# Optimization experiments

Measured on AMD Instinct MI355X. Metric: run time of the kernel, lower is better.

Reference implementation:

```python
import jax, jax.numpy as jnp
import numpy as np

N_NODES = 100000

def _sage(x, src, tgt, Wl, bl, Wr):
    # PyG SAGEConv (mean aggr): out = lin_l(mean_{j in N(i)} x_j) + lin_r(x_i)
    msg = x[src]                                             # [E, F] gather
    s = jax.ops.segment_sum(msg, tgt, num_segments=N_NODES)  # [N, F]
    cnt = jax.ops.segment_sum(jnp.ones((src.shape[0], 1), x.dtype), tgt, num_segments=N_NODES)
    agg = s / jnp.maximum(cnt, 1.0)
    return agg @ Wl + bl + x @ Wr


def setup_inputs() -> dict:
    key = jax.random.key(0)
    ks = jax.random.split(key, 16)
    node_dim, edge_dim, hidden = 128, 16, 64
    E = 1000000
    x = jax.random.normal(ks[0], (N_NODES, node_dim), jnp.float32)
    edge_index = jax.random.randint(ks[1], (2, E), 0, N_NODES, jnp.int64)
    edge_attr = jax.random.normal(ks[2], (E, edge_dim), jnp.float32)
    def lin(k, fi, fo, scale=None):
        s = scale if scale is not None else 1.0 / np.sqrt(fi)
        return jax.random.uniform(k, (fi, fo), jnp.float32, -s, s)
    return {
        "x": x, "edge_index": edge_index, "edge_attr": edge_attr,
        # edge MLP: Linear(16,64) -> ReLU -> Linear(64,64)
        "We1": lin(ks[3], edge_dim, hidden), "be1": jnp.zeros((hidden,), jnp.float32),
        "We2": lin(ks[4], hidden, hidden),   "be2": jnp.zeros((hidden,), jnp.float32),
        # SAGEConv 0: lin_l (with bias, on aggregated) + lin_r (no bias, on root)
        "Wl0": lin(ks[5], node_dim, hidden), "bl0": jnp.zeros((hidden,), jnp.float32),
        "Wr0": lin(ks[6], node_dim, hidden),
        # SAGEConv 1
        "Wl1": lin(ks[7], hidden, hidden), "bl1": jnp.zeros((hidden,), jnp.float32),
        "Wr1": lin(ks[8], hidden, hidden),
        # output MLP: Linear(64,64) -> ReLU -> (Dropout eval=id) -> Linear(64,1)
        "Wo1": lin(ks[9], hidden, hidden), "bo1": jnp.zeros((hidden,), jnp.float32),
        "Wo2": lin(ks[10], hidden, 1),     "bo2": jnp.zeros((1,), jnp.float32),
    }


def reference(x, edge_index, edge_attr, We1, be1, We2, be2,
              Wl0, bl0, Wr0, Wl1, bl1, Wr1, Wo1, bo1, Wo2, bo2):
    src, tgt = edge_index[0], edge_index[1]
    # edge MLP (dropout in eval mode = identity)
    ea = jax.nn.relu(edge_attr @ We1 + be1) @ We2 + be2       # [E, H]
    # two SAGE layers with ReLU
    h = jax.nn.relu(_sage(x, src, tgt, Wl0, bl0, Wr0))        # [N, H]
    h = jax.nn.relu(_sage(h, src, tgt, Wl1, bl1, Wr1))        # [N, H]
    # per-edge features: gather both endpoints + edge embedding
    ef = h[src] + h[tgt] + ea                                 # [E, H]
    out = jax.nn.relu(ef @ Wo1 + bo1) @ Wo2 + bo2             # [E, 1]
    return jax.nn.sigmoid(out[:, 0])                          # [E]
```

## Files before the change

kernel.cpp:

```cpp
#include <hip/hip_runtime.h>
#include <math.h>

typedef __attribute__((ext_vector_type(8))) short short8;
typedef __attribute__((ext_vector_type(4))) float f32x4;

static __device__ __forceinline__ unsigned short f2bf(float f) {
  union { float f; unsigned int u; } x; x.f = f;
  unsigned int r = x.u + 0x7fffu + ((x.u >> 16) & 1u);
  return (unsigned short)(r >> 16);
}
static __device__ __forceinline__ float bf2f(unsigned int u) {
  union { unsigned int u; float f; } x; x.u = u << 16; return x.f;
}

__global__ void k_flag(const unsigned int* __restrict__ w, int nSample,
                       unsigned int* __restrict__ flag) {
  __shared__ unsigned int red[256];
  unsigned int v = 0;
  for (int i = threadIdx.x; i < nSample; i += 256) v |= w[2 * i + 1];
  red[threadIdx.x] = v;
  __syncthreads();
  for (int s = 128; s > 0; s >>= 1) {
    if (threadIdx.x < s) red[threadIdx.x] |= red[threadIdx.x + s];
    __syncthreads();
  }
  if (threadIdx.x == 0) flag[0] = red[0];
}

__global__ void k_decode(const unsigned int* __restrict__ w,
                         const unsigned int* __restrict__ flag, int E,
                         int* __restrict__ src, int* __restrict__ tgt,
                         int* __restrict__ posin, int* __restrict__ deg) {
  int e = blockIdx.x * 256 + threadIdx.x;
  if (e >= E) return;
  int s, t;
  if (flag[0]) { s = (int)w[e]; t = (int)w[E + e]; }
  else         { s = (int)w[2 * e]; t = (int)w[2 * (E + e)]; }
  src[e] = s;
  tgt[e] = t;
  posin[e] = atomicAdd(deg + t, 1);
}

__global__ __launch_bounds__(256) void k_scan1(const int* __restrict__ deg,
                                               int* __restrict__ bsum) {
  __shared__ int wsum[4];
  const int tid = threadIdx.x, lane = tid & 63, wid = tid >> 6;
  const int base = blockIdx.x * 2048 + tid * 8;
  int4 v0 = *(const int4*)(deg + base);
  int4 v1 = *(const int4*)(deg + base + 4);
  int s = v0.x + v0.y + v0.z + v0.w + v1.x + v1.y + v1.z + v1.w;
#pragma unroll
  for (int off = 1; off < 64; off <<= 1) s += __shfl_xor(s, off, 64);
  if (lane == 0) wsum[wid] = s;
  __syncthreads();
  if (tid == 0) bsum[blockIdx.x] = wsum[0] + wsum[1] + wsum[2] + wsum[3];
}

__global__ void k_scan2(const int* __restrict__ bsum, int* __restrict__ boff,
                        int nB, int* __restrict__ rowptrN) {
  int lane = threadIdx.x;
  int v = (lane < nB) ? bsum[lane] : 0;
  int incl = v;
#pragma unroll
  for (int off = 1; off < 64; off <<= 1) {
    int t = __shfl_up(incl, off, 64);
    if (lane >= off) incl += t;
  }
  if (lane < nB) boff[lane] = incl - v;
  if (lane == 63) *rowptrN = incl;
}

__global__ __launch_bounds__(256) void k_scan3(const int* __restrict__ deg,
                                               const int* __restrict__ boff,
                                               int* __restrict__ rowptr) {
  __shared__ int wsum[4];
  const int tid = threadIdx.x, lane = tid & 63, wid = tid >> 6;
  const int base = blockIdx.x * 2048 + tid * 8;
  int4 v0 = *(const int4*)(deg + base);
  int4 v1 = *(const int4*)(deg + base + 4);
  int e[8] = {v0.x, v0.y, v0.z, v0.w, v1.x, v1.y, v1.z, v1.w};
  int s = e[0] + e[1] + e[2] + e[3] + e[4] + e[5] + e[6] + e[7];
  int incl = s;
#pragma unroll
  for (int off = 1; off < 64; off <<= 1) {
    int t = __shfl_up(incl, off, 64);
    if (lane >= off) incl += t;
  }
  if (lane == 63) wsum[wid] = incl;
  __syncthreads();
  int run = boff[blockIdx.x] + (incl - s);
  for (int w = 0; w < wid; ++w) run += wsum[w];
  int o[8];
#pragma unroll
  for (int i = 0; i < 8; ++i) { o[i] = run; run += e[i]; }
  *(int4*)(rowptr + base) = make_int4(o[0], o[1], o[2], o[3]);
  *(int4*)(rowptr + base + 4) = make_int4(o[4], o[5], o[6], o[7]);
}

__global__ void k_fill(const int* __restrict__ src, const int* __restrict__ tgt,
                       const int* __restrict__ posin,
                       const int* __restrict__ rowptr,
                       int* __restrict__ csrc, int E) {
  int e = blockIdx.x * 256 + threadIdx.x;
  if (e >= E) return;
  csrc[rowptr[tgt[e]] + posin[e]] = src[e];
}

template <int K>
__global__ void k_prep2(const float* __restrict__ W0,
                        const float* __restrict__ W1,
                        unsigned short* __restrict__ WnT) {
  int idx = blockIdx.x * 256 + threadIdx.x;
  if (idx >= 128 * K) return;
  int n = idx / K, k = idx % K;
  float v = (n < 64) ? W0[(size_t)k * 64 + n] : W1[(size_t)k * 64 + (n - 64)];
  WnT[idx] = f2bf(v);
}

template <int K, bool BF16IN, int NTILES>
__global__ __launch_bounds__(256) void k_ngemm(
    const void* __restrict__ Xv, const unsigned short* __restrict__ WnT,
    unsigned short* __restrict__ Y0, unsigned short* __restrict__ Y1, int N) {
  constexpr int STR = K + 8;
  constexpr int NC = K / 32;
  __shared__ unsigned short sX[64 * STR];
  const int tid = threadIdx.x;
  const int wv = tid >> 6, lane = tid & 63;
  const int m = lane & 15, q = lane >> 4;
  const int row0 = blockIdx.x * 64;

  short8 bB[NTILES][NC];
#pragma unroll
  for (int ct = 0; ct < NTILES; ++ct)
#pragma unroll
    for (int c = 0; c < NC; ++c) {
      int n = (NTILES == 2) ? (wv * 32 + ct * 16 + m) : (wv * 16 + m);
      bB[ct][c] = *(const short8*)(WnT + (size_t)n * K + c * 32 + q * 8);
    }

#pragma unroll
  for (int i = 0; i < K / 16; ++i) {
    int f = tid + 256 * i;
    int r = f / (K / 4);
    int c4 = f % (K / 4);
    int rr = row0 + r; if (rr >= N) rr = N - 1;
    uint2 pk;
    if constexpr (BF16IN) {
      pk = *(const uint2*)((const unsigned short*)Xv + (size_t)rr * K + c4 * 4);
    } else {
      float4 v = *(const float4*)((const float*)Xv + (size_t)rr * K + c4 * 4);
      pk.x = (unsigned int)f2bf(v.x) | ((unsigned int)f2bf(v.y) << 16);
      pk.y = (unsigned int)f2bf(v.z) | ((unsigned int)f2bf(v.w) << 16);
    }
    *(uint2*)(sX + r * STR + c4 * 4) = pk;
  }
  __syncthreads();

  f32x4 acc[4][NTILES];
#pragma unroll
  for (int rt = 0; rt < 4; ++rt)
#pragma unroll
    for (int ct = 0; ct < NTILES; ++ct)
#pragma unroll
      for (int r = 0; r < 4; ++r) acc[rt][ct][r] = 0.f;

#pragma unroll
  for (int c = 0; c < NC; ++c) {
    short8 a[4];
#pragma unroll
    for (int rt = 0; rt < 4; ++rt)
      a[rt] = *(const short8*)(sX + (rt * 16 + m) * STR + c * 32 + q * 8);
#pragma unroll
    for (int rt = 0; rt < 4; ++rt)
#pragma unroll
      for (int ct = 0; ct < NTILES; ++ct)
        acc[rt][ct] = __builtin_amdgcn_mfma_f32_16x16x32_bf16(a[rt], bB[ct][c], acc[rt][ct], 0, 0, 0);
  }

#pragma unroll
  for (int rt = 0; rt < 4; ++rt)
#pragma unroll
    for (int ct = 0; ct < NTILES; ++ct) {
      unsigned short* Yw;
      int n;
      if constexpr (NTILES == 2) {
        Yw = (wv < 2) ? Y0 : Y1;
        n = (wv & 1) * 32 + ct * 16 + m;
      } else {
        Yw = Y0;
        n = wv * 16 + m;
      }
#pragma unroll
      for (int reg = 0; reg < 4; ++reg) {
        int row = row0 + rt * 16 + q * 4 + reg;
        if (row < N) Yw[(size_t)row * 64 + n] = f2bf(acc[rt][ct][reg]);
      }
    }
}

__global__ __launch_bounds__(256) void k_prep(
    const float* __restrict__ We2, const float* __restrict__ Wo1,
    const float* __restrict__ be2, const float* __restrict__ bo1,
    const float* __restrict__ We1,
    unsigned short* __restrict__ W25T, unsigned short* __restrict__ We1T,
    unsigned short* __restrict__ Wo1T, float* __restrict__ cvec) {
  __shared__ float sA[4096];
  __shared__ float sB[4096];
  int tid = threadIdx.x;
  for (int i = tid; i < 1024; i += 256) {
    *(float4*)&sA[i * 4] = *(const float4*)(We2 + i * 4);
    *(float4*)&sB[i * 4] = *(const float4*)(Wo1 + i * 4);
  }
  __syncthreads();
  for (int idx = tid; idx < 4096; idx += 256) {
    int n = idx >> 6, k = idx & 63;
    float s = 0.f;
#pragma unroll 8
    for (int mm = 0; mm < 64; ++mm) s = fmaf(sA[k * 64 + mm], sB[mm * 64 + n], s);
    W25T[idx] = f2bf(s);
    Wo1T[idx] = f2bf(sB[k * 64 + n]);
  }
  for (int idx = tid; idx < 2048; idx += 256) {
    int n = idx >> 5, k = idx & 31;
    We1T[n * 32 + k] = (k < 16) ? f2bf(We1[k * 64 + n]) : (unsigned short)0;
  }
  if (tid < 64) {
    float s = bo1[tid];
#pragma unroll 8
    for (int mm = 0; mm < 64; ++mm) s = fmaf(be2[mm], sB[mm * 64 + tid], s);
    cvec[tid] = s;
  }
}

__global__ __launch_bounds__(256) void k_agg(
    const unsigned short* __restrict__ Y, const int* __restrict__ rowptr,
    const int* __restrict__ csrc, const float* __restrict__ bias,
    const unsigned short* __restrict__ Yr, unsigned short* __restrict__ H,
    int N) {
  int node = (blockIdx.x * 256 + threadIdx.x) >> 6;
  if (node >= N) return;
  const int lane = threadIdx.x & 63;
  const int c4 = lane & 15, rr = lane >> 4;
  int beg = rowptr[node], end = rowptr[node + 1];
  float a0 = 0.f, a1 = 0.f, a2 = 0.f, a3 = 0.f;
  float b0 = 0.f, b1 = 0.f, b2 = 0.f, b3 = 0.f;
  for (int e = beg; e < end; e += 8) {
    int e0 = e + rr, e1 = e + 4 + rr;
    if (e0 < end) {
      int s = csrc[e0];
      uint2 v = *(const uint2*)(Y + (size_t)s * 64 + c4 * 4);
      a0 += bf2f(v.x & 0xffffu); a1 += bf2f(v.x >> 16);
      a2 += bf2f(v.y & 0xffffu); a3 += bf2f(v.y >> 16);
    }
    if (e1 < end) {
      int s = csrc[e1];
      uint2 v = *(const uint2*)(Y + (size_t)s * 64 + c4 * 4);
      b0 += bf2f(v.x & 0xffffu); b1 += bf2f(v.x >> 16);
      b2 += bf2f(v.y & 0xffffu); b3 += bf2f(v.y >> 16);
    }
  }
  a0 += b0; a1 += b1; a2 += b2; a3 += b3;
#pragma unroll
  for (int msk = 16; msk <= 32; msk <<= 1) {
    a0 += __shfl_xor(a0, msk, 64);
    a1 += __shfl_xor(a1, msk, 64);
    a2 += __shfl_xor(a2, msk, 64);
    a3 += __shfl_xor(a3, msk, 64);
  }
  if (rr == 0) {
    float cdeg = (float)(end - beg);
    if (cdeg < 1.f) cdeg = 1.f;
    float inv = 1.f / cdeg;
    float4 bv = *(const float4*)(bias + c4 * 4);
    uint2 yv = *(const uint2*)(Yr + (size_t)node * 64 + c4 * 4);
    float o0 = fmaxf(a0 * inv + bv.x + bf2f(yv.x & 0xffffu), 0.f);
    float o1 = fmaxf(a1 * inv + bv.y + bf2f(yv.x >> 16), 0.f);
    float o2 = fmaxf(a2 * inv + bv.z + bf2f(yv.y & 0xffffu), 0.f);
    float o3 = fmaxf(a3 * inv + bv.w + bf2f(yv.y >> 16), 0.f);
    uint2 pk;
    pk.x = (unsigned int)f2bf(o0) | ((unsigned int)f2bf(o1) << 16);
    pk.y = (unsigned int)f2bf(o2) | ((unsigned int)f2bf(o3) << 16);
    *(uint2*)(H + (size_t)node * 64 + c4 * 4) = pk;
  }
}

#define T1_STRIDE 72
#define G_STRIDE 68
__global__ __launch_bounds__(256) void k_edge3(
    const float* __restrict__ eattr, const int* __restrict__ src,
    const int* __restrict__ tgt, const unsigned short* __restrict__ Gb,
    const unsigned short* __restrict__ We1T,
    const unsigned short* __restrict__ W25T,
    const float* __restrict__ cvec, const float* __restrict__ be1,
    const float* __restrict__ Wo2, const float* __restrict__ bo2,
    float* __restrict__ out, int E, int nT, int nWaves) {
  __shared__ unsigned short sT1a[4][16 * T1_STRIDE];
  __shared__ float sGa[4][16 * G_STRIDE];
  const int tid = threadIdx.x;
  const int wid = tid >> 6, lane = tid & 63;
  const int m = lane & 15, q = lane >> 4;
  unsigned short* sT1 = sT1a[wid];
  float* sG = sGa[wid];

  short8 bWe1[4], bW25[4][2];
  float cv[4], wo2v[4], be1v[4];
#pragma unroll
  for (int nt = 0; nt < 4; ++nt) {
    int n = nt * 16 + m;
    bWe1[nt] = *(const short8*)(We1T + n * 32 + q * 8);
    bW25[nt][0] = *(const short8*)(W25T + n * 64 + q * 8);
    bW25[nt][1] = *(const short8*)(W25T + n * 64 + 32 + q * 8);
    cv[nt] = cvec[n];
    wo2v[nt] = Wo2[n];
    be1v[nt] = be1[n];
  }
  const float b_out = bo2[0];
  const short8 zfrag = {};

  int t = blockIdx.x * 4 + wid;
  if (t >= nT) return;
  int il = t * 16 + m; if (il >= E) il = E - 1;
  int my_idx = (lane < 16) ? src[il] : ((lane < 32) ? tgt[il] : 0);

  while (true) {
    const int base = t * 16;
    const int tn = t + nWaves;
    const bool last = (tn >= nT);
    const int tc = last ? t : tn;

    int il_n = tc * 16 + m; if (il_n >= E) il_n = E - 1;
    int idx_n = (lane < 16) ? src[il_n] : ((lane < 32) ? tgt[il_n] : 0);

    int rs[4], rt[4];
#pragma unroll
    for (int r = 0; r < 4; ++r) {
      rs[r] = __shfl(my_idx, q * 4 + r, 64);
      rt[r] = __shfl(my_idx, 16 + q * 4 + r, 64);
    }
    uint2 sv[4], tv[4];
#pragma unroll
    for (int r = 0; r < 4; ++r) {
      sv[r] = *(const uint2*)(Gb + (size_t)rs[r] * 64 + m * 4);
      tv[r] = *(const uint2*)(Gb + (size_t)rt[r] * 64 + m * 4);
    }

    int er = base + m; if (er >= E) er = E - 1;
    const float* ep = eattr + (size_t)er * 16 + (q & 1) * 8;
    float4 e0 = *(const float4*)ep;
    float4 e1 = *(const float4*)(ep + 4);
    short8 aEA;
    {
      union { short8 s; unsigned int u[4]; } ua;
      ua.u[0] = (unsigned int)f2bf(e0.x) | ((unsigned int)f2bf(e0.y) << 16);
      ua.u[1] = (unsigned int)f2bf(e0.z) | ((unsigned int)f2bf(e0.w) << 16);
      ua.u[2] = (unsigned int)f2bf(e1.x) | ((unsigned int)f2bf(e1.y) << 16);
      ua.u[3] = (unsigned int)f2bf(e1.z) | ((unsigned int)f2bf(e1.w) << 16);
      aEA = (q < 2) ? ua.s : zfrag;
    }

    f32x4 t1[4];
#pragma unroll
    for (int nt = 0; nt < 4; ++nt) {
      f32x4 cinit; cinit[0] = be1v[nt]; cinit[1] = be1v[nt];
      cinit[2] = be1v[nt]; cinit[3] = be1v[nt];
      t1[nt] = __builtin_amdgcn_mfma_f32_16x16x32_bf16(aEA, bWe1[nt], cinit, 0, 0, 0);
    }
#pragma unroll
    for (int nt = 0; nt < 4; ++nt)
#pragma unroll
      for (int r = 0; r < 4; ++r)
        sT1[(q * 4 + r) * T1_STRIDE + nt * 16 + m] = f2bf(fmaxf(t1[nt][r], 0.f));
    short8 aT0 = *(short8*)(sT1 + m * T1_STRIDE + q * 8);
    short8 aT1 = *(short8*)(sT1 + m * T1_STRIDE + 32 + q * 8);

#pragma unroll
    for (int r = 0; r < 4; ++r) {
      f32x4 g;
      g[0] = bf2f(sv[r].x & 0xffffu) + bf2f(tv[r].x & 0xffffu);
      g[1] = bf2f(sv[r].x >> 16)     + bf2f(tv[r].x >> 16);
      g[2] = bf2f(sv[r].y & 0xffffu) + bf2f(tv[r].y & 0xffffu);
      g[3] = bf2f(sv[r].y >> 16)     + bf2f(tv[r].y >> 16);
      *(f32x4*)(sG + (q * 4 + r) * G_STRIDE + m * 4) = g;
    }

    f32x4 acc[4];
#pragma unroll
    for (int nt = 0; nt < 4; ++nt)
#pragma unroll
      for (int r = 0; r < 4; ++r)
        acc[nt][r] = cv[nt] + sG[(q * 4 + r) * G_STRIDE + nt * 16 + m];
#pragma unroll
    for (int nt = 0; nt < 4; ++nt) {
      acc[nt] = __builtin_amdgcn_mfma_f32_16x16x32_bf16(aT0, bW25[nt][0], acc[nt], 0, 0, 0);
      acc[nt] = __builtin_amdgcn_mfma_f32_16x16x32_bf16(aT1, bW25[nt][1], acc[nt], 0, 0, 0);
    }

    float p[4];
#pragma unroll
    for (int r = 0; r < 4; ++r) {
      p[r] = fmaxf(acc[0][r], 0.f) * wo2v[0] + fmaxf(acc[1][r], 0.f) * wo2v[1] +
             fmaxf(acc[2][r], 0.f) * wo2v[2] + fmaxf(acc[3][r], 0.f) * wo2v[3];
    }
#pragma unroll
    for (int msk = 1; msk <= 8; msk <<= 1) {
#pragma unroll
      for (int r = 0; r < 4; ++r) p[r] += __shfl_xor(p[r], msk, 64);
    }
    if (m == 0) {
#pragma unroll
      for (int r = 0; r < 4; ++r) {
        int row = base + q * 4 + r;
        if (row < E) out[row] = 1.f / (1.f + __expf(-(p[r] + b_out)));
      }
    }

    if (last) break;
    t = tn; my_idx = idx_n;
  }
}

extern "C" void kernel_launch(void* const* d_in, const int* in_sizes, int n_in,
                              void* d_out, int out_size, void* d_ws, size_t ws_size,
                              hipStream_t stream) {
  const float* x     = (const float*)d_in[0];
  const unsigned int* eidx = (const unsigned int*)d_in[1];
  const float* eattr = (const float*)d_in[2];
  const float* We1 = (const float*)d_in[3];
  const float* be1 = (const float*)d_in[4];
  const float* We2 = (const float*)d_in[5];
  const float* be2 = (const float*)d_in[6];
  const float* Wl0 = (const float*)d_in[7];
  const float* bl0 = (const float*)d_in[8];
  const float* Wr0 = (const float*)d_in[9];
  const float* Wl1 = (const float*)d_in[10];
  const float* bl1 = (const float*)d_in[11];
  const float* Wr1 = (const float*)d_in[12];
  const float* Wo1 = (const float*)d_in[13];
  const float* bo1 = (const float*)d_in[14];
  const float* Wo2 = (const float*)d_in[15];
  const float* bo2 = (const float*)d_in[16];

  const int N = in_sizes[0] / 128;
  const int E = in_sizes[2] / 16;
  const int padN = (N + 2047) & ~2047;
  const int nB = padN / 2048;
  float* out = (float*)d_out;

  char* ws = (char*)d_ws;
  size_t off = 0;
  auto alloc = [&](size_t bytes) {
    char* p = ws + off;
    off += (bytes + 255) & ~(size_t)255;
    return p;
  };
  unsigned int* flag = (unsigned int*)alloc(256);
  int* src    = (int*)alloc((size_t)E * 4);
  int* tgt    = (int*)alloc((size_t)E * 4);
  int* posin  = (int*)alloc((size_t)E * 4);
  int* deg    = (int*)alloc((size_t)padN * 4);
  int* rowptr = (int*)alloc((size_t)(padN + 64) * 4);
  int* bsum   = (int*)alloc(64 * 4);
  int* boff   = (int*)alloc(64 * 4);
  int* csrc   = (int*)alloc((size_t)E * 4);
  unsigned short* Hb = (unsigned short*)alloc((size_t)N * 64 * 2);
  unsigned short* Yl = (unsigned short*)alloc((size_t)N * 64 * 2);
  unsigned short* Yr = (unsigned short*)alloc((size_t)N * 64 * 2);
  unsigned short* Gb = (unsigned short*)alloc((size_t)N * 64 * 2);
  unsigned short* W25T = (unsigned short*)alloc(64 * 64 * 2);
  unsigned short* We1T = (unsigned short*)alloc(64 * 32 * 2);
  unsigned short* Wo1T = (unsigned short*)alloc(64 * 64 * 2);
  unsigned short* WnT0 = (unsigned short*)alloc(128 * 128 * 2);
  unsigned short* WnT1 = (unsigned short*)alloc(128 * 64 * 2);
  float* cvec = (float*)alloc(64 * 4);
  (void)ws_size; (void)n_in; (void)out_size;

  hipMemsetAsync(deg, 0, (size_t)padN * 4, stream);

  k_flag<<<1, 256, 0, stream>>>(eidx, 8192, flag);
  k_decode<<<(E + 255) / 256, 256, 0, stream>>>(eidx, flag, E, src, tgt, posin, deg);
  k_scan1<<<nB, 256, 0, stream>>>(deg, bsum);
  k_scan2<<<1, 64, 0, stream>>>(bsum, boff, nB, rowptr + N);
  k_scan3<<<nB, 256, 0, stream>>>(deg, boff, rowptr);
  k_fill<<<(E + 255) / 256, 256, 0, stream>>>(src, tgt, posin, rowptr, csrc, E);
  k_prep<<<1, 256, 0, stream>>>(We2, Wo1, be2, bo1, We1, W25T, We1T, Wo1T, cvec);
  k_prep2<128><<<64, 256, 0, stream>>>(Wl0, Wr0, WnT0);
  k_prep2<64><<<32, 256, 0, stream>>>(Wl1, Wr1, WnT1);

  const int gB = (N + 63) / 64;
  k_ngemm<128, false, 2><<<gB, 256, 0, stream>>>(x, WnT0, Yl, Yr, N);
  k_agg<<<(N + 3) / 4, 256, 0, stream>>>(Yl, rowptr, csrc, bl0, Yr, Hb, N);

  k_ngemm<64, true, 2><<<gB, 256, 0, stream>>>(Hb, WnT1, Yl, Yr, N);
  k_agg<<<(N + 3) / 4, 256, 0, stream>>>(Yl, rowptr, csrc, bl1, Yr, Hb, N);

  k_ngemm<64, true, 1><<<gB, 256, 0, stream>>>(Hb, Wo1T, Gb, nullptr, N);

  const int nT = (E + 15) / 16;
  const int blocks = 2048;
  k_edge3<<<blocks, 256, 0, stream>>>(eattr, src, tgt, Gb, We1T, W25T, cvec,
                                      be1, Wo2, bo2, out, E, nT, blocks * 4);
}
```

Before: 455.8 us.

## Pre-convert edge attributes to bf16 in decode and merge setup kernels

Edge attributes are converted to bf16 inside the decode kernel through a grid-stride pass into a new workspace buffer. The edge kernel then loads packed bf16 fragments directly instead of loading and converting fp32. The degree memset is folded into a multi-block k_flag, and the three weight-prep kernels are merged into one 97-block kernel, which removes launches. The edge kernel grid also grows from 2048 to 3072 blocks. The cost is an extra full read of edge_attr plus a bf16 write, which may outweigh the smaller edge-kernel read.

```diff
diff --git a/kernel.cpp b/kernel.cpp
--- a/kernel.cpp
+++ b/kernel.cpp
@@ -14,7 +14,13 @@
 }
 
 __global__ void k_flag(const unsigned int* __restrict__ w, int nSample,
-                       unsigned int* __restrict__ flag) {
+                       unsigned int* __restrict__ flag,
+                       int* __restrict__ deg, int padN) {
+  int4* d4 = (int4*)deg;
+  int n4 = padN >> 2;
+  for (int i = blockIdx.x * 256 + threadIdx.x; i < n4; i += gridDim.x * 256)
+    d4[i] = make_int4(0, 0, 0, 0);
+  if (blockIdx.x != 0) return;
   __shared__ unsigned int red[256];
   unsigned int v = 0;
   for (int i = threadIdx.x; i < nSample; i += 256) v |= w[2 * i + 1];
@@ -29,9 +35,20 @@
 
 __global__ void k_decode(const unsigned int* __restrict__ w,
                          const unsigned int* __restrict__ flag, int E,
+                         const float4* __restrict__ ef,
+                         uint2* __restrict__ eb,
                          int* __restrict__ src, int* __restrict__ tgt,
                          int* __restrict__ posin, int* __restrict__ deg) {
-  int e = blockIdx.x * 256 + threadIdx.x;
+  int gid = blockIdx.x * 256 + threadIdx.x;
+  int stride = gridDim.x * 256;
+  for (int i = gid; i < E * 4; i += stride) {
+    float4 v = ef[i];
+    uint2 pk;
+    pk.x = (unsigned int)f2bf(v.x) | ((unsigned int)f2bf(v.y) << 16);
+    pk.y = (unsigned int)f2bf(v.z) | ((unsigned int)f2bf(v.w) << 16);
+    eb[i] = pk;
+  }
+  int e = gid;
   if (e >= E) return;
   int s, t;
   if (flag[0]) { s = (int)w[e]; t = (int)w[E + e]; }
@@ -57,7 +74,7 @@
 }
 
 __global__ void k_scan2(const int* __restrict__ bsum, int* __restrict__ boff,
-                        int nB, int* __restrict__ rowptrN) {
+                        int nB) {
   int lane = threadIdx.x;
   int v = (lane < nB) ? bsum[lane] : 0;
   int incl = v;
@@ -67,7 +84,6 @@
     if (lane >= off) incl += t;
   }
   if (lane < nB) boff[lane] = incl - v;
-  if (lane == 63) *rowptrN = incl;
 }
 
 __global__ __launch_bounds__(256) void k_scan3(const int* __restrict__ deg,
@@ -106,15 +122,53 @@
   csrc[rowptr[tgt[e]] + posin[e]] = src[e];
 }
 
-template <int K>
-__global__ void k_prep2(const float* __restrict__ W0,
-                        const float* __restrict__ W1,
-                        unsigned short* __restrict__ WnT) {
-  int idx = blockIdx.x * 256 + threadIdx.x;
-  if (idx >= 128 * K) return;
-  int n = idx / K, k = idx % K;
-  float v = (n < 64) ? W0[(size_t)k * 64 + n] : W1[(size_t)k * 64 + (n - 64)];
-  WnT[idx] = f2bf(v);
+__global__ __launch_bounds__(256) void k_prepall(
+    const float* __restrict__ We2, const float* __restrict__ Wo1,
+    const float* __restrict__ be2, const float* __restrict__ bo1,
+    const float* __restrict__ We1,
+    const float* __restrict__ Wl0, const float* __restrict__ Wr0,
+    const float* __restrict__ Wl1, const float* __restrict__ Wr1,
+    unsigned short* __restrict__ W25T, unsigned short* __restrict__ We1T,
+    unsigned short* __restrict__ Wo1T, float* __restrict__ cvec,
+    unsigned short* __restrict__ WnT0, unsigned short* __restrict__ WnT1) {
+  const int tid = threadIdx.x;
+  if (blockIdx.x == 0) {
+    __shared__ float sA[4096];
+    __shared__ float sB[4096];
+    for (int i = tid; i < 1024; i += 256) {
+      *(float4*)&sA[i * 4] = *(const float4*)(We2 + i * 4);
+      *(float4*)&sB[i * 4] = *(const float4*)(Wo1 + i * 4);
+    }
+    __syncthreads();
+    for (int idx = tid; idx < 4096; idx += 256) {
+      int n = idx >> 6, k = idx & 63;
+      float s = 0.f;
+#pragma unroll 8
+      for (int mm = 0; mm < 64; ++mm) s = fmaf(sA[k * 64 + mm], sB[mm * 64 + n], s);
+      W25T[idx] = f2bf(s);
+      Wo1T[idx] = f2bf(sB[k * 64 + n]);
+    }
+    for (int idx = tid; idx < 2048; idx += 256) {
+      int n = idx >> 5, k = idx & 31;
+      We1T[n * 32 + k] = (k < 16) ? f2bf(We1[k * 64 + n]) : (unsigned short)0;
+    }
+    if (tid < 64) {
+      float s = bo1[tid];
+#pragma unroll 8
+      for (int mm = 0; mm < 64; ++mm) s = fmaf(be2[mm], sB[mm * 64 + tid], s);
+      cvec[tid] = s;
+    }
+  } else if (blockIdx.x <= 64) {
+    int idx = (blockIdx.x - 1) * 256 + tid;
+    int n = idx >> 7, k = idx & 127;
+    float v = (n < 64) ? Wl0[(size_t)k * 64 + n] : Wr0[(size_t)k * 64 + (n - 64)];
+    WnT0[idx] = f2bf(v);
+  } else {
+    int idx = (blockIdx.x - 65) * 256 + tid;
+    int n = idx >> 6, k = idx & 63;
+    float v = (n < 64) ? Wl1[(size_t)k * 64 + n] : Wr1[(size_t)k * 64 + (n - 64)];
+    WnT1[idx] = f2bf(v);
+  }
 }
 
 template <int K, bool BF16IN, int NTILES>
@@ -196,40 +250,6 @@
         if (row < N) Yw[(size_t)row * 64 + n] = f2bf(acc[rt][ct][reg]);
       }
     }
-}
-
-__global__ __launch_bounds__(256) void k_prep(
-    const float* __restrict__ We2, const float* __restrict__ Wo1,
-    const float* __restrict__ be2, const float* __restrict__ bo1,
-    const float* __restrict__ We1,
-    unsigned short* __restrict__ W25T, unsigned short* __restrict__ We1T,
-    unsigned short* __restrict__ Wo1T, float* __restrict__ cvec) {
-  __shared__ float sA[4096];
-  __shared__ float sB[4096];
-  int tid = threadIdx.x;
-  for (int i = tid; i < 1024; i += 256) {
-    *(float4*)&sA[i * 4] = *(const float4*)(We2 + i * 4);
-    *(float4*)&sB[i * 4] = *(const float4*)(Wo1 + i * 4);
-  }
-  __syncthreads();
-  for (int idx = tid; idx < 4096; idx += 256) {
-    int n = idx >> 6, k = idx & 63;
-    float s = 0.f;
-#pragma unroll 8
-    for (int mm = 0; mm < 64; ++mm) s = fmaf(sA[k * 64 + mm], sB[mm * 64 + n], s);
-    W25T[idx] = f2bf(s);
-    Wo1T[idx] = f2bf(sB[k * 64 + n]);
-  }
-  for (int idx = tid; idx < 2048; idx += 256) {
-    int n = idx >> 5, k = idx & 31;
-    We1T[n * 32 + k] = (k < 16) ? f2bf(We1[k * 64 + n]) : (unsigned short)0;
-  }
-  if (tid < 64) {
-    float s = bo1[tid];
-#pragma unroll 8
-    for (int mm = 0; mm < 64; ++mm) s = fmaf(be2[mm], sB[mm * 64 + tid], s);
-    cvec[tid] = s;
-  }
 }
 
 __global__ __launch_bounds__(256) void k_agg(
@@ -287,7 +307,7 @@
 #define T1_STRIDE 72
 #define G_STRIDE 68
 __global__ __launch_bounds__(256) void k_edge3(
-    const float* __restrict__ eattr, const int* __restrict__ src,
+    const unsigned short* __restrict__ EAb, const int* __restrict__ src,
     const int* __restrict__ tgt, const unsigned short* __restrict__ Gb,
     const unsigned short* __restrict__ We1T,
     const unsigned short* __restrict__ W25T,
@@ -345,18 +365,8 @@
     }
 
     int er = base + m; if (er >= E) er = E - 1;
-    const float* ep = eattr + (size_t)er * 16 + (q & 1) * 8;
-    float4 e0 = *(const float4*)ep;
-    float4 e1 = *(const float4*)(ep + 4);
-    short8 aEA;
-    {
-      union { short8 s; unsigned int u[4]; } ua;
-      ua.u[0] = (unsigned int)f2bf(e0.x) | ((unsigned int)f2bf(e0.y) << 16);
-      ua.u[1] = (unsigned int)f2bf(e0.z) | ((unsigned int)f2bf(e0.w) << 16);
-      ua.u[2] = (unsigned int)f2bf(e1.x) | ((unsigned int)f2bf(e1.y) << 16);
-      ua.u[3] = (unsigned int)f2bf(e1.z) | ((unsigned int)f2bf(e1.w) << 16);
-      aEA = (q < 2) ? ua.s : zfrag;
-    }
+    short8 aEA = zfrag;
+    if (q < 2) aEA = *(const short8*)(EAb + (size_t)er * 16 + (q & 1) * 8);
 
     f32x4 t1[4];
 #pragma unroll
@@ -462,6 +472,7 @@
   int* bsum   = (int*)alloc(64 * 4);
   int* boff   = (int*)alloc(64 * 4);
   int* csrc   = (int*)alloc((size_t)E * 4);
+  unsigned short* EAb = (unsigned short*)alloc((size_t)E * 16 * 2);
   unsigned short* Hb = (unsigned short*)alloc((size_t)N * 64 * 2);
   unsigned short* Yl = (unsigned short*)alloc((size_t)N * 64 * 2);
   unsigned short* Yr = (unsigned short*)alloc((size_t)N * 64 * 2);
@@ -474,17 +485,15 @@
   float* cvec = (float*)alloc(64 * 4);
   (void)ws_size; (void)n_in; (void)out_size;
 
-  hipMemsetAsync(deg, 0, (size_t)padN * 4, stream);
-
-  k_flag<<<1, 256, 0, stream>>>(eidx, 8192, flag);
-  k_decode<<<(E + 255) / 256, 256, 0, stream>>>(eidx, flag, E, src, tgt, posin, deg);
+  k_flag<<<64, 256, 0, stream>>>(eidx, 8192, flag, deg, padN);
+  k_decode<<<(E + 255) / 256, 256, 0, stream>>>(
+      eidx, flag, E, (const float4*)eattr, (uint2*)EAb, src, tgt, posin, deg);
   k_scan1<<<nB, 256, 0, stream>>>(deg, bsum);
-  k_scan2<<<1, 64, 0, stream>>>(bsum, boff, nB, rowptr + N);
+  k_scan2<<<1, 64, 0, stream>>>(bsum, boff, nB);
   k_scan3<<<nB, 256, 0, stream>>>(deg, boff, rowptr);
   k_fill<<<(E + 255) / 256, 256, 0, stream>>>(src, tgt, posin, rowptr, csrc, E);
-  k_prep<<<1, 256, 0, stream>>>(We2, Wo1, be2, bo1, We1, W25T, We1T, Wo1T, cvec);
-  k_prep2<128><<<64, 256, 0, stream>>>(Wl0, Wr0, WnT0);
-  k_prep2<64><<<32, 256, 0, stream>>>(Wl1, Wr1, WnT1);
+  k_prepall<<<97, 256, 0, stream>>>(We2, Wo1, be2, bo1, We1, Wl0, Wr0, Wl1, Wr1,
+                                    W25T, We1T, Wo1T, cvec, WnT0, WnT1);
 
   const int gB = (N + 63) / 64;
   k_ngemm<128, false, 2><<<gB, 256, 0, stream>>>(x, WnT0, Yl, Yr, N);
@@ -496,7 +505,7 @@
   k_ngemm<64, true, 1><<<gB, 256, 0, stream>>>(Hb, Wo1T, Gb, nullptr, N);
 
   const int nT = (E + 15) / 16;
-  const int blocks = 2048;
-  k_edge3<<<blocks, 256, 0, stream>>>(eattr, src, tgt, Gb, We1T, W25T, cvec,
+  const int blocks = 3072;
+  k_edge3<<<blocks, 256, 0, stream>>>(EAb, src, tgt, Gb, We1T, W25T, cvec,
                                       be1, Wo2, bo2, out, E, nT, blocks * 4);
 }
```

After: 456.4 us. No clear change (+0.1%).
